# Kernel tuning notes

Measured on AMD Instinct MI355X. Metric: run time of the kernel, lower is better.

Reference implementation:

```python
import jax, jax.numpy as jnp
import numpy as np
import math

HEADS = 8
GROUPS = 4
PW = 2  # pooling_window
EPS = 1e-5


def group_norm(x, w, b, groups=GROUPS):
    # x: (B, C, *spatial); normalize over (C//groups, *spatial) per group
    B, C = x.shape[0], x.shape[1]
    xs = x.reshape(B, groups, -1)
    mu = xs.mean(-1, keepdims=True)
    var = xs.var(-1, keepdims=True)
    xs = (xs - mu) / jnp.sqrt(var + EPS)
    shape = (1, C) + (1,) * (x.ndim - 2)
    return xs.reshape(x.shape) * w.reshape(shape) + b.reshape(shape)


def cst_pool(x, pw=PW):
    # x: (B, C, Tq, Ts) with Ts = h*w + 1 (class token first); avg-pool spatial part
    cls_tok, sp = x[..., :1], x[..., 1:]
    B, C, Tq, S = sp.shape
    h = math.isqrt(S)
    sp = sp.reshape(B, C, Tq, h // pw, pw, h // pw, pw).mean(axis=(4, 6))
    return jnp.concatenate([cls_tok, sp.reshape(B, C, Tq, -1)], axis=-1)


def conv1x1(x, w):
    # w: (O, C); x: (B, C, Tq, Ts)
    return jnp.einsum('oc,bcqs->boqs', w, x)


def interp_bilinear_ac(m, n):
    # bilinear resize to (n, n), align_corners=True; m: (B, H, W) float
    def axis_interp(x, size, axis, L):
        c = jnp.linspace(0.0, L - 1.0, size)
        i0 = jnp.floor(c).astype(jnp.int32)
        i1 = jnp.minimum(i0 + 1, L - 1)
        f = (c - i0).astype(x.dtype)
        x0 = jnp.take(x, i0, axis=axis)
        x1 = jnp.take(x, i1, axis=axis)
        shape = [1] * x.ndim
        shape[axis] = size
        f = f.reshape(shape)
        return x0 * (1 - f) + x1 * f
    B, H, W = m.shape
    return axis_interp(axis_interp(m, n, 1, H), n, 2, W)


def setup_inputs() -> dict:
    key = jax.random.key(0)
    ks = jax.random.split(key, 8)
    B, Cin, Tq, Ts = 4, 128, 256, 257
    Cout = 512
    hidden = Cout // 2  # 256
    H = W = 256
    s = 0.05
    return {
        'corr_tokens': jax.random.normal(ks[0], (B, Cin, Tq, Ts), jnp.float32),
        's_masks': jax.random.randint(ks[1], (B, H, W), 0, 2, jnp.int32),
        'W_sc': jax.random.normal(ks[2], (Cout, Cin), jnp.float32) * s,
        'gn_sc_w': jnp.ones((Cout,), jnp.float32),
        'gn_sc_b': jnp.zeros((Cout,), jnp.float32),
        'W_qkv': jax.random.normal(ks[3], (3 * hidden, Cin), jnp.float32) * s,
        'b_qkv': jax.random.normal(ks[4], (3 * hidden,), jnp.float32) * s,
        'gn1_w': jnp.ones((hidden,), jnp.float32),
        'gn1_b': jnp.zeros((hidden,), jnp.float32),
        'W_agg': jax.random.normal(ks[5], (Cout, hidden), jnp.float32) * s,
        'gn2_w': jnp.ones((Cout,), jnp.float32),
        'gn2_b': jnp.zeros((Cout,), jnp.float32),
        'gn_out_w': jnp.ones((Cout,), jnp.float32),
        'gn_out_b': jnp.zeros((Cout,), jnp.float32),
    }


def reference(corr_tokens, s_masks, W_sc, gn_sc_w, gn_sc_b, W_qkv, b_qkv,
              gn1_w, gn1_b, W_agg, gn2_w, gn2_b, gn_out_w, gn_out_b):
    B, _, Tq, Ts = corr_tokens.shape
    hidden = W_qkv.shape[0] // 3
    E = hidden // HEADS

    # short_cut branch: conv1x1 -> CSTPooling -> GroupNorm -> ReLU
    residual = jax.nn.relu(group_norm(cst_pool(conv1x1(corr_tokens, W_sc)), gn_sc_w, gn_sc_b))

    # qkv projection
    qkv = conv1x1(corr_tokens, W_qkv) + b_qkv[None, :, None, None]
    qkv = qkv.reshape(B, 3, HEADS, E, Tq, Ts)  # channel order (x, g, e)
    q, k, v = qkv[:, 0], qkv[:, 1], qkv[:, 2]

    # pool queries over support-spatial dim: (B,G,E,Tq,Ts) -> (B,G,E,Tq,Td)
    q = cst_pool(q.reshape(B, hidden, Tq, Ts))
    Td = q.shape[-1]
    q = q.reshape(B, HEADS, E, Tq, Td)

    # per-query masked attention
    attn = jnp.einsum('bgeqd,bgeqs->bgqds', q, k)  # (B,G,Tq,Td,Ts)
    sdim = math.isqrt(Ts - 1)
    m = interp_bilinear_ac(jnp.minimum(s_masks, 1).astype(jnp.float32), sdim)
    m = m.reshape(B, 1, 1, 1, sdim * sdim)
    attn_seg = jnp.where(m == 0, jnp.float32(-1e9), attn[..., 1:])
    attn = jnp.concatenate([attn[..., :1], attn_seg], axis=-1)
    attn = jax.nn.softmax(attn, axis=-1)
    out = jnp.einsum('bgqds,bgeqs->bgeqd', attn, v).reshape(B, hidden, Tq, Td)

    # agg: GN -> ReLU -> conv1x1 -> GN -> ReLU
    out = jax.nn.relu(group_norm(out, gn1_w, gn1_b))
    out = conv1x1(out, W_agg)
    out = jax.nn.relu(group_norm(out, gn2_w, gn2_b))

    return group_norm(out + residual, gn_out_w, gn_out_b)
```

## Files before the change

### kernel.cpp

```cpp
#include <hip/hip_runtime.h>
#include <stdint.h>

#define NB    4
#define TQ    256
#define TS    257
#define TD    65
#define NPIX  16640
#define NPADQ 264
#define NPAD  67584
#define COUT  512
#define HID   256

typedef __attribute__((ext_vector_type(8))) short bf16x8;
typedef __attribute__((ext_vector_type(4))) float f32x4;

__device__ __forceinline__ float bf2f(unsigned short u) {
    union { unsigned int i; float f; } v; v.i = ((unsigned int)u) << 16; return v.f;
}
__device__ __forceinline__ unsigned short f2bf(float x) {
    union { float f; unsigned int i; } v; v.f = x;
    unsigned int r = v.i + 0x7fffu + ((v.i >> 16) & 1u);
    return (unsigned short)(r >> 16);
}

__device__ __forceinline__ float2 gn_params(const float* st, int bg, float invcnt) {
    float mu  = st[bg * 2] * invcnt;
    float var = st[bg * 2 + 1] * invcnt - mu * mu;
    float2 r; r.x = mu; r.y = rsqrtf(var + 1e-5f); return r;
}

__global__ void wprep_kernel(const float* __restrict__ wq, const float* __restrict__ wsc,
                             const float* __restrict__ wagg, unsigned short* __restrict__ wb) {
    int i = blockIdx.x * 256 + threadIdx.x;
    float v;
    if (i < 98304) v = wq[i];
    else if (i < 163840) v = wsc[i - 98304];
    else v = wagg[i - 163840];
    wb[i] = f2bf(v);
}

__global__ void mask_kernel(const int* __restrict__ sm, float* __restrict__ bias) {
    int b = blockIdx.x; int t = threadIdx.x;
    if (t >= 272) return;
    float v;
    if (t == 0) v = 0.0f;
    else if (t <= 256) {
        int s = t - 1; int i = s >> 4, j = s & 15;
        v = (sm[(size_t)b * 65536 + i * 17 * 256 + j * 17] != 0) ? 0.0f : -1e9f;
    } else v = -1e9f;
    bias[b * 272 + t] = v;
}

__global__ __launch_bounds__(256) void tpool_kernel(
    const float* __restrict__ corr,
    unsigned short* __restrict__ corrT,
    unsigned short* __restrict__ corrpT)
{
    int q = blockIdx.x, ch = blockIdx.y, b = blockIdx.z;
    int t = threadIdx.x;
    __shared__ unsigned short sT[264 * 66];

    {
        int laneT = t & 63; int crow = t >> 6;
        for (int c = crow; c < 64; c += 4) {
            const float* src = corr + (((size_t)b * 128 + ch * 64 + c) * 256 + q) * 257;
            for (int s = laneT; s < 257; s += 64) sT[s * 66 + c] = f2bf(src[s]);
        }
    }
    for (int idx = t; idx < 7 * 66; idx += 256) {
        int s = 257 + idx / 66, c = idx % 66;
        sT[s * 66 + c] = 0;
    }
    __syncthreads();

    {
        unsigned int* dst = (unsigned int*)corrT;
        size_t base = (size_t)b * (NPAD * 64) + (size_t)q * (264 * 64) + ch * 32;
        for (int idx = t; idx < 264 * 32; idx += 256) {
            int s = idx >> 5, cu = idx & 31;
            unsigned int v = (unsigned int)sT[s * 66 + 2 * cu] |
                             ((unsigned int)sT[s * 66 + 2 * cu + 1] << 16);
            dst[base + (size_t)s * 64 + cu] = v;
        }
    }
    {
        unsigned int* dst = (unsigned int*)corrpT;
        size_t base = (size_t)b * (NPIX * 64) + (size_t)q * (65 * 64) + ch * 32;
        for (int idx = t; idx < 65 * 32; idx += 256) {
            int d = idx >> 5, cu = idx & 31;
            float x0, x1;
            if (d == 0) {
                x0 = bf2f(sT[0 * 66 + 2 * cu]); x1 = bf2f(sT[0 * 66 + 2 * cu + 1]);
            } else {
                int dd = d - 1; int i = dd >> 3, j = dd & 7;
                int s = 1 + i * 32 + j * 2;
                int c0 = 2 * cu, c1 = 2 * cu + 1;
                x0 = 0.25f * (bf2f(sT[s*66+c0]) + bf2f(sT[(s+1)*66+c0]) +
                              bf2f(sT[(s+16)*66+c0]) + bf2f(sT[(s+17)*66+c0]));
                x1 = 0.25f * (bf2f(sT[s*66+c1]) + bf2f(sT[(s+1)*66+c1]) +
                              bf2f(sT[(s+16)*66+c1]) + bf2f(sT[(s+17)*66+c1]));
            }
            unsigned int v = (unsigned int)f2bf(x0) | ((unsigned int)f2bf(x1) << 16);
            dst[base + (size_t)d * 64 + cu] = v;
        }
    }
}

template<int MODE, int KT>
__global__ __launch_bounds__(256) void mgemm_kernel(
    const unsigned short* __restrict__ X,
    const unsigned short* __restrict__ Wb,
    int Nn,
    float* __restrict__ Yf,
    unsigned short* __restrict__ Y16,
    unsigned short* __restrict__ kb,
    unsigned short* __restrict__ vb,
    const float* __restrict__ bias,
    const float* __restrict__ st, const float* __restrict__ gw, const float* __restrict__ gb,
    float invcnt)
{
    int b  = blockIdx.z;
    int n0 = blockIdx.x * 128;
    int m0 = blockIdx.y * 128;
    int t = threadIdx.x;
    int w = t >> 6, lane = t & 63;
    int lm = lane & 15, lg = lane >> 4;
    int wn = (w & 1) * 64, wm = (w >> 1) * 64;

    __shared__ __align__(16) unsigned short sX[16384];
    __shared__ __align__(16) unsigned short sW[16384];

    f32x4 acc[4][4];
    #pragma unroll
    for (int i = 0; i < 4; i++)
        #pragma unroll
        for (int j = 0; j < 4; j++) { acc[i][j][0]=0.f; acc[i][j][1]=0.f; acc[i][j][2]=0.f; acc[i][j][3]=0.f; }

    for (int kc = 0; kc < KT / 128; kc++) {
        for (int i = t; i < 2048; i += 256) {
            int r_ = i >> 4, kq = i & 15;
            uint4 xv = *(const uint4*)&X[((size_t)b * Nn + n0 + r_) * KT + kc * 128 + (kq << 3)];
            if (MODE == 3) {
                union { uint4 v; unsigned short us[8]; } u; u.v = xv;
                int c0 = kc * 128 + (kq << 3);
                float2 p = gn_params(st, b * 4 + (c0 >> 6), invcnt);
                #pragma unroll
                for (int jj = 0; jj < 8; jj++) {
                    int cc = c0 + jj;
                    float v = bf2f(u.us[jj]);
                    v = fmaxf((v - p.x) * p.y * gw[cc] + gb[cc], 0.0f);
                    u.us[jj] = f2bf(v);
                }
                xv = u.v;
            }
            *(uint4*)&sX[r_ * 128 + ((kq ^ (r_ & 15)) << 3)] = xv;
            uint4 wv = *(const uint4*)&Wb[((size_t)(m0 + r_)) * KT + kc * 128 + (kq << 3)];
            *(uint4*)&sW[r_ * 128 + ((kq ^ (r_ & 15)) << 3)] = wv;
        }
        __syncthreads();
        #pragma unroll
        for (int kk = 0; kk < 4; kk++) {
            int kg = (kk << 2) | lg;
            bf16x8 af[4], bw[4];
            #pragma unroll
            for (int ii = 0; ii < 4; ii++)
                af[ii] = *(const bf16x8*)&sX[(wn + ii * 16 + lm) * 128 + ((kg ^ lm) << 3)];
            #pragma unroll
            for (int jj = 0; jj < 4; jj++)
                bw[jj] = *(const bf16x8*)&sW[(wm + jj * 16 + lm) * 128 + ((kg ^ lm) << 3)];
            #pragma unroll
            for (int ii = 0; ii < 4; ii++)
                #pragma unroll
                for (int jj = 0; jj < 4; jj++) {
                    if (MODE == 0)
                        acc[ii][jj] = __builtin_amdgcn_mfma_f32_16x16x32_bf16(bw[jj], af[ii], acc[ii][jj], 0,0,0);
                    else
                        acc[ii][jj] = __builtin_amdgcn_mfma_f32_16x16x32_bf16(af[ii], bw[jj], acc[ii][jj], 0,0,0);
                }
        }
        __syncthreads();
    }

    if (MODE == 0) {
        #pragma unroll
        for (int ii = 0; ii < 4; ii++) {
            int n = n0 + wn + ii * 16 + lm;
            #pragma unroll
            for (int jj = 0; jj < 4; jj++) {
                int mb = m0 + wm + jj * 16 + lg * 4;
                union { unsigned short us[4]; uint2 v; } pk;
                #pragma unroll
                for (int r = 0; r < 4; r++) pk.us[r] = f2bf(acc[ii][jj][r] + bias[mb + r]);
                *(uint2*)&Y16[((size_t)b * NPIX + n) * 256 + mb] = pk.v;
            }
        }
    } else if (MODE == 1) {
        if (m0 < 256) {
            #pragma unroll
            for (int ii = 0; ii < 4; ii++) {
                #pragma unroll
                for (int r = 0; r < 4; r++) {
                    unsigned int np = (unsigned int)(n0 + wn + ii * 16 + lg * 4 + r);
                    unsigned int qq = np / 264u;
                    unsigned int s  = np - qq * 264u;
                    #pragma unroll
                    for (int jj = 0; jj < 4; jj++) {
                        int m = m0 + wm + jj * 16 + lm;
                        int gch = m >> 5, e = m & 31;
                        kb[(((size_t)(b * 8 + gch) * 256 + qq) * 264 + s) * 32 + e] =
                            f2bf(acc[ii][jj][r] + bias[m]);
                    }
                }
            }
        } else {
            #pragma unroll
            for (int ii = 0; ii < 4; ii++) {
                int nb = n0 + wn + ii * 16 + lg * 4;
                #pragma unroll
                for (int jj = 0; jj < 4; jj++) {
                    int m = m0 + wm + jj * 16 + lm;
                    int mv = m - 256;
                    union { unsigned short us[4]; uint2 v; } pk;
                    #pragma unroll
                    for (int r = 0; r < 4; r++) pk.us[r] = f2bf(acc[ii][jj][r] + bias[m]);
                    *(uint2*)&vb[((size_t)b * 256 + mv) * NPAD + nb] = pk.v;
                }
            }
        }
    } else {
        #pragma unroll
        for (int ii = 0; ii < 4; ii++) {
            int nb = n0 + wn + ii * 16 + lg * 4;
            #pragma unroll
            for (int jj = 0; jj < 4; jj++) {
                int m = m0 + wm + jj * 16 + lm;
                *(f32x4*)&Yf[((size_t)b * COUT + m) * NPIX + nb] = acc[ii][jj];
            }
        }
    }
}

__global__ __launch_bounds__(320, 3) void attn_kernel(
    const unsigned short* __restrict__ kb,
    const unsigned short* __restrict__ vb,
    const unsigned short* __restrict__ qpT,
    const float* __restrict__ bias272,
    unsigned short* __restrict__ attT)
{
    int g = blockIdx.x, q = blockIdx.y, b = blockIdx.z;
    int t = threadIdx.x;
    int w = t >> 6, lane = t & 63;
    int lm = lane & 15, lg = lane >> 4;

    __shared__ __align__(16) unsigned short sP[23040];
    unsigned short* sPw = sP + w * 4608;

    int d = w * 16 + lm;
    int dc = d < 64 ? d : 64;
    bf16x8 qa = *(const bf16x8*)&qpT[((size_t)b * NPIX + q * 65 + dc) * 256 + g * 32 + lg * 8];
    if (d >= TD) { bf16x8 z = {}; qa = z; }

    size_t kb0 = ((size_t)(b * 8 + g) * 256 + q) * (264 * 32);
    const unsigned short* kp = kb + kb0 + (size_t)lm * 32 + lg * 8;
    bf16x8 kf[17];
    #pragma unroll
    for (int tt = 0; tt < 17; tt++)
        kf[tt] = *(const bf16x8*)&kp[tt * 512];

    f32x4 zero4 = {0.f, 0.f, 0.f, 0.f};
    f32x4 c[17];
    #pragma unroll
    for (int tt = 0; tt < 17; tt++)
        c[tt] = __builtin_amdgcn_mfma_f32_16x16x32_bf16(kf[tt], qa, zero4, 0, 0, 0);

    size_t vb0 = ((size_t)b * 256 + g * 32) * NPAD + (size_t)q * 264;
    const unsigned short* vp = vb + vb0 + (size_t)lm * NPAD + lg * 8;
    bf16x8 vf0[9], vf1[9];
    #pragma unroll
    for (int kk = 0; kk < 9; kk++) {
        vf0[kk] = *(const bf16x8*)&vp[kk * 32];
        vf1[kk] = *(const bf16x8*)&vp[16 * NPAD + kk * 32];
    }

    const float* bp = bias272 + b * 272 + lg * 4;
    #pragma unroll
    for (int tt = 0; tt < 17; tt++) {
        f32x4 bf = *(const f32x4*)&bp[tt * 16];
        c[tt][0] += bf[0]; c[tt][1] += bf[1]; c[tt][2] += bf[2]; c[tt][3] += bf[3];
    }

    f32x4 mv = c[0];
    #pragma unroll
    for (int tt = 1; tt < 17; tt++) {
        mv[0] = fmaxf(mv[0], c[tt][0]); mv[1] = fmaxf(mv[1], c[tt][1]);
        mv[2] = fmaxf(mv[2], c[tt][2]); mv[3] = fmaxf(mv[3], c[tt][3]);
    }
    float mx = fmaxf(fmaxf(mv[0], mv[1]), fmaxf(mv[2], mv[3]));
    mx = fmaxf(mx, __shfl_xor(mx, 16));
    mx = fmaxf(mx, __shfl_xor(mx, 32));
    float sm = 0.f;
    #pragma unroll
    for (int tt = 0; tt < 17; tt++) {
        #pragma unroll
        for (int r = 0; r < 4; r++) { float e_ = __expf(c[tt][r] - mx); c[tt][r] = e_; sm += e_; }
    }
    sm += __shfl_xor(sm, 16);
    sm += __shfl_xor(sm, 32);
    float inv = 1.0f / sm;

    #pragma unroll
    for (int tt = 0; tt < 17; tt++) {
        union { unsigned short us[4]; uint2 v; } pk;
        #pragma unroll
        for (int r = 0; r < 4; r++) pk.us[r] = f2bf(c[tt][r] * inv);
        int sg = tt * 2 + (lg >> 1);
        int off = lm * 288 + ((sg ^ (lm & 3)) << 3) + (lg & 1) * 4;
        *(uint2*)&sPw[off] = pk.v;
    }
    if (lg < 2) {
        int sg = 34 + lg;
        uint4 z4 = {0u, 0u, 0u, 0u};
        *(uint4*)&sPw[lm * 288 + ((sg ^ (lm & 3)) << 3)] = z4;
    }

    f32x4 o0 = zero4, o1 = zero4;
    #pragma unroll
    for (int kk = 0; kk < 9; kk++) {
        int kg = kk * 4 + lg;
        bf16x8 pa = *(const bf16x8*)&sPw[lm * 288 + ((kg ^ (lm & 3)) << 3)];
        o0 = __builtin_amdgcn_mfma_f32_16x16x32_bf16(pa, vf0[kk], o0, 0, 0, 0);
        o1 = __builtin_amdgcn_mfma_f32_16x16x32_bf16(pa, vf1[kk], o1, 0, 0, 0);
    }
    #pragma unroll
    for (int r = 0; r < 4; r++) {
        int dd = w * 16 + lg * 4 + r;
        if (dd < TD) {
            size_t nn = (size_t)b * NPIX + q * 65 + dd;
            attT[nn * 256 + g * 32 + lm]      = f2bf(o0[r]);
            attT[nn * 256 + g * 32 + 16 + lm] = f2bf(o1[r]);
        }
    }
}

__global__ void stats1_kernel(const unsigned short* __restrict__ attT, float* __restrict__ st) {
    int b = blockIdx.y;
    int t = threadIdx.x;
    int e8 = t & 31, g = e8 >> 3;
    int lane = t & 63;
    float s = 0.f, ss = 0.f;
    for (int r = blockIdx.x * 8 + (t >> 5); r < NPIX; r += gridDim.x * 8) {
        union { uint4 v; unsigned short us[8]; } u;
        u.v = *(const uint4*)&attT[((size_t)b * NPIX + r) * 256 + e8 * 8];
        #pragma unroll
        for (int j = 0; j < 8; j++) { float x = bf2f(u.us[j]); s += x; ss += x * x; }
    }
    s += __shfl_down(s, 32); ss += __shfl_down(ss, 32);
    s += __shfl_down(s, 4);  ss += __shfl_down(ss, 4);
    s += __shfl_down(s, 2);  ss += __shfl_down(ss, 2);
    s += __shfl_down(s, 1);  ss += __shfl_down(ss, 1);
    if (lane < 32 && (lane & 7) == 0) {
        atomicAdd(&st[(b * 4 + g) * 2],     s);
        atomicAdd(&st[(b * 4 + g) * 2 + 1], ss);
    }
}

__global__ void stats_kernel(const float* __restrict__ x, float* __restrict__ st, int Cg) {
    size_t len = (size_t)Cg * NPIX;
    size_t base = (size_t)blockIdx.y * len;
    const float4* x4 = reinterpret_cast<const float4*>(x + base);
    size_t len4 = len >> 2;
    float s = 0.f, ss = 0.f;
    for (size_t i = (size_t)blockIdx.x * blockDim.x + threadIdx.x; i < len4;
         i += (size_t)gridDim.x * blockDim.x) {
        float4 v = x4[i];
        s  += v.x + v.y + v.z + v.w;
        ss += v.x * v.x + v.y * v.y + v.z * v.z + v.w * v.w;
    }
    #pragma unroll
    for (int o = 32; o > 0; o >>= 1) { s += __shfl_down(s, o, 64); ss += __shfl_down(ss, o, 64); }
    __shared__ float red[4][2];
    int wid = threadIdx.x >> 6, lane = threadIdx.x & 63;
    if (lane == 0) { red[wid][0] = s; red[wid][1] = ss; }
    __syncthreads();
    if (threadIdx.x == 0) {
        float S  = red[0][0] + red[1][0] + red[2][0] + red[3][0];
        float SS = red[0][1] + red[1][1] + red[2][1] + red[3][1];
        atomicAdd(&st[blockIdx.y * 2],     S);
        atomicAdd(&st[blockIdx.y * 2 + 1], SS);
    }
}

__global__ void z_kernel(float* __restrict__ out, const float* __restrict__ scr,
                         const float* __restrict__ st2, const float* __restrict__ stsc,
                         const float* __restrict__ g2w, const float* __restrict__ g2b,
                         const float* __restrict__ gsw, const float* __restrict__ gsb)
{
    const float invcnt = 1.0f / (128.0f * NPIX);
    size_t total4 = (size_t)NB * COUT * (NPIX / 4);
    float4* o4 = reinterpret_cast<float4*>(out);
    const float4* s4 = reinterpret_cast<const float4*>(scr);
    for (size_t i = (size_t)blockIdx.x * blockDim.x + threadIdx.x; i < total4;
         i += (size_t)gridDim.x * blockDim.x) {
        size_t flat = i * 4;
        int c = (int)((flat / NPIX) % COUT);
        int b = (int)(flat / ((size_t)COUT * NPIX));
        int bg = b * 4 + (c >> 7);
        float2 p2 = gn_params(st2,  bg, invcnt);
        float2 ps = gn_params(stsc, bg, invcnt);
        float w2 = g2w[c] * p2.y, b2 = g2b[c] - p2.x * p2.y * g2w[c];
        float wsc = gsw[c] * ps.y, bsc = gsb[c] - ps.x * ps.y * gsw[c];
        float4 a = o4[i], r = s4[i], z;
        z.x = fmaxf(a.x * w2 + b2, 0.f) + fmaxf(r.x * wsc + bsc, 0.f);
        z.y = fmaxf(a.y * w2 + b2, 0.f) + fmaxf(r.y * wsc + bsc, 0.f);
        z.z = fmaxf(a.z * w2 + b2, 0.f) + fmaxf(r.z * wsc + bsc, 0.f);
        z.w = fmaxf(a.w * w2 + b2, 0.f) + fmaxf(r.w * wsc + bsc, 0.f);
        o4[i] = z;
    }
}

__global__ void norm_kernel(float* __restrict__ out, const float* __restrict__ st3,
                            const float* __restrict__ gw, const float* __restrict__ gb)
{
    const float invcnt = 1.0f / (128.0f * NPIX);
    size_t total4 = (size_t)NB * COUT * (NPIX / 4);
    float4* o4 = reinterpret_cast<float4*>(out);
    for (size_t i = (size_t)blockIdx.x * blockDim.x + threadIdx.x; i < total4;
         i += (size_t)gridDim.x * blockDim.x) {
        size_t flat = i * 4;
        int c = (int)((flat / NPIX) % COUT);
        int b = (int)(flat / ((size_t)COUT * NPIX));
        int bg = b * 4 + (c >> 7);
        float2 p = gn_params(st3, bg, invcnt);
        float w_ = gw[c] * p.y, b_ = gb[c] - p.x * p.y * gw[c];
        float4 a = o4[i], z;
        z.x = a.x * w_ + b_; z.y = a.y * w_ + b_; z.z = a.z * w_ + b_; z.w = a.w * w_ + b_;
        o4[i] = z;
    }
}

extern "C" void kernel_launch(void* const* d_in, const int* in_sizes, int n_in,
                              void* d_out, int out_size, void* d_ws, size_t ws_size,
                              hipStream_t stream) {
    (void)in_sizes; (void)n_in; (void)out_size; (void)ws_size;
    const float* corr     = (const float*)d_in[0];
    const int*   smask    = (const int*)  d_in[1];
    const float* W_sc     = (const float*)d_in[2];
    const float* gn_sc_w  = (const float*)d_in[3];
    const float* gn_sc_b  = (const float*)d_in[4];
    const float* W_qkv    = (const float*)d_in[5];
    const float* b_qkv    = (const float*)d_in[6];
    const float* gn1_w    = (const float*)d_in[7];
    const float* gn1_b    = (const float*)d_in[8];
    const float* W_agg    = (const float*)d_in[9];
    const float* gn2_w    = (const float*)d_in[10];
    const float* gn2_b    = (const float*)d_in[11];
    const float* gn_out_w = (const float*)d_in[12];
    const float* gn_out_b = (const float*)d_in[13];
    float* out = (float*)d_out;

    unsigned short* ws = (unsigned short*)d_ws;
    unsigned short* corrT  = ws;
    unsigned short* kbuf   = corrT  + (size_t)34603008;
    unsigned short* vbuf   = kbuf   + (size_t)69206016;
    unsigned short* corrpT = vbuf   + (size_t)69206016;
    unsigned short* qpT    = corrpT + (size_t)8519680;
    unsigned short* attT   = qpT    + (size_t)17039360;
    unsigned short* wbuf   = attT   + (size_t)17039360;
    float* bias  = (float*)(wbuf + (size_t)294912);
    float* stats = bias + 1088;
    float* scr   = (float*)d_ws;
    float* st_sc = stats, *st1 = stats + 32, *st2 = stats + 64, *st3 = stats + 96;

    const float inv1 = 1.0f / (64.0f * (float)NPIX);

    hipMemsetAsync(stats, 0, 128 * sizeof(float), stream);
    wprep_kernel<<<dim3(1152), dim3(256), 0, stream>>>(W_qkv, W_sc, W_agg, wbuf);
    mask_kernel<<<dim3(NB), dim3(320), 0, stream>>>(smask, bias);
    tpool_kernel<<<dim3(TQ, 2, NB), dim3(256), 0, stream>>>(corr, corrT, corrpT);
    mgemm_kernel<0,128><<<dim3(130, 2, NB), dim3(256), 0, stream>>>(
        corrpT, wbuf, NPIX, nullptr, qpT, nullptr, nullptr, b_qkv,
        nullptr, nullptr, nullptr, 0.f);
    mgemm_kernel<1,128><<<dim3(528, 4, NB), dim3(256), 0, stream>>>(
        corrT, wbuf + 32768, NPAD, nullptr, nullptr, kbuf, vbuf, b_qkv + 256,
        nullptr, nullptr, nullptr, 0.f);
    attn_kernel<<<dim3(8, TQ, NB), dim3(320), 0, stream>>>(kbuf, vbuf, qpT, bias, attT);
    stats1_kernel<<<dim3(208, NB), dim3(256), 0, stream>>>(attT, st1);
    mgemm_kernel<3,256><<<dim3(130, 4, NB), dim3(256), 0, stream>>>(
        attT, wbuf + 163840, NPIX, out, nullptr, nullptr, nullptr, nullptr,
        st1, gn1_w, gn1_b, inv1);
    stats_kernel<<<dim3(64, 16), dim3(256), 0, stream>>>(out, st2, 128);
    mgemm_kernel<2,128><<<dim3(130, 4, NB), dim3(256), 0, stream>>>(
        corrpT, wbuf + 98304, NPIX, scr, nullptr, nullptr, nullptr, nullptr,
        nullptr, nullptr, nullptr, 0.f);
    stats_kernel<<<dim3(64, 16), dim3(256), 0, stream>>>(scr, st_sc, 128);
    z_kernel<<<dim3(4096), dim3(256), 0, stream>>>(out, scr, st2, st_sc, gn2_w, gn2_b, gn_sc_w, gn_sc_b);
    stats_kernel<<<dim3(64, 16), dim3(256), 0, stream>>>(out, st3, 128);
    norm_kernel<<<dim3(4096), dim3(256), 0, stream>>>(out, st3, gn_out_w, gn_out_b);
}
```

Before: 1.059 ms.

## Stage K/V tiles through LDS via direct global-to-LDS loads, keep P in registers

The attention kernel used to have every wave load its own K and V fragments straight from global memory into registers. It now loads the shared K/V tile once per block into swizzled LDS using global_load_lds, with out-of-range rows read from a zero pad buffer. The softmax probabilities are no longer staged in LDS: they are packed with v_cvt_pk_bf16_f32 and rearranged across lanes with permlane32_swap and shuffles. Normalisation is deferred until after the PV product. This cuts redundant global loads across the five waves and the LDS round-trip for P, at the cost of a block-wide barrier and a dependence on a zero region inside corrT.

After: 982.4 us. 1.08x faster.

```diff
diff --git a/kernel.cpp b/kernel.cpp
--- a/kernel.cpp
+++ b/kernel.cpp
@@ -27,6 +27,13 @@
     float mu  = st[bg * 2] * invcnt;
     float var = st[bg * 2 + 1] * invcnt - mu * mu;
     float2 r; r.x = mu; r.y = rsqrtf(var + 1e-5f); return r;
+}
+
+__device__ __forceinline__ void gld_lds16(const void* g, void* l) {
+    __builtin_amdgcn_global_load_lds(
+        (const __attribute__((address_space(1))) unsigned int*)(size_t)g,
+        (__attribute__((address_space(3))) unsigned int*)(unsigned int)(size_t)l,
+        16, 0, 0);
 }
 
 __global__ void wprep_kernel(const float* __restrict__ wq, const float* __restrict__ wsc,
@@ -244,6 +251,7 @@
     const unsigned short* __restrict__ kb,
     const unsigned short* __restrict__ vb,
     const unsigned short* __restrict__ qpT,
+    const unsigned short* __restrict__ zpad,
     const float* __restrict__ bias272,
     unsigned short* __restrict__ attT)
 {
@@ -252,8 +260,8 @@
     int w = t >> 6, lane = t & 63;
     int lm = lane & 15, lg = lane >> 4;
 
-    __shared__ __align__(16) unsigned short sP[23040];
-    unsigned short* sPw = sP + w * 4608;
+    __shared__ __align__(16) unsigned short sbuf[17920];
+    const int VB = 8704;
 
     int d = w * 16 + lm;
     int dc = d < 64 ? d : 64;
@@ -261,25 +269,35 @@
     if (d >= TD) { bf16x8 z = {}; qa = z; }
 
     size_t kb0 = ((size_t)(b * 8 + g) * 256 + q) * (264 * 32);
-    const unsigned short* kp = kb + kb0 + (size_t)lm * 32 + lg * 8;
-    bf16x8 kf[17];
-    #pragma unroll
-    for (int tt = 0; tt < 17; tt++)
-        kf[tt] = *(const bf16x8*)&kp[tt * 512];
+    size_t vrow0 = (size_t)b * 256 + g * 32;
+    for (int cc = w; cc < 35; cc += 5) {
+        unsigned o = cc * 1024 + lane * 16;
+        const unsigned short* src;
+        if (cc < 17) {
+            unsigned mr = o >> 8, sl = (o >> 4) & 15;
+            unsigned lam = (o & ~0xF0u) | ((sl ^ (mr & 15)) << 4);
+            src = (lam < 16896u) ? (kb + kb0 + (lam >> 1)) : zpad;
+        } else {
+            unsigned ov = o - 17408u;
+            unsigned mr = ov >> 8, sl = (ov >> 4) & 15;
+            unsigned lam = (ov & ~0xF0u) | ((sl ^ (mr & 15)) << 4);
+            unsigned kk = lam >> 11, ch = (lam >> 6) & 31;
+            unsigned s = kk * 32 + ((lam >> 4) & 3) * 8;
+            src = (s < 264u) ? (vb + ((vrow0 + ch) * NPAD + (size_t)q * 264 + s)) : zpad;
+        }
+        gld_lds16(src, &sbuf[cc * 512]);
+    }
+    asm volatile("s_waitcnt vmcnt(0)" ::: "memory");
+    __syncthreads();
 
     f32x4 zero4 = {0.f, 0.f, 0.f, 0.f};
     f32x4 c[17];
-    #pragma unroll
-    for (int tt = 0; tt < 17; tt++)
-        c[tt] = __builtin_amdgcn_mfma_f32_16x16x32_bf16(kf[tt], qa, zero4, 0, 0, 0);
-
-    size_t vb0 = ((size_t)b * 256 + g * 32) * NPAD + (size_t)q * 264;
-    const unsigned short* vp = vb + vb0 + (size_t)lm * NPAD + lg * 8;
-    bf16x8 vf0[9], vf1[9];
-    #pragma unroll
-    for (int kk = 0; kk < 9; kk++) {
-        vf0[kk] = *(const bf16x8*)&vp[kk * 32];
-        vf1[kk] = *(const bf16x8*)&vp[16 * NPAD + kk * 32];
+    int sl0 = ((lm & 3) << 2) | lg;
+    #pragma unroll
+    for (int tt = 0; tt < 17; tt++) {
+        int mr = tt * 4 + (lm >> 2);
+        bf16x8 kf = *(const bf16x8*)&sbuf[mr * 128 + ((sl0 ^ (mr & 15)) << 3)];
+        c[tt] = __builtin_amdgcn_mfma_f32_16x16x32_bf16(kf, qa, zero4, 0, 0, 0);
     }
 
     const float* bp = bias272 + b * 272 + lg * 4;
@@ -308,36 +326,46 @@
     sm += __shfl_xor(sm, 32);
     float inv = 1.0f / sm;
 
+    unsigned plo[17], phi[17];
     #pragma unroll
     for (int tt = 0; tt < 17; tt++) {
-        union { unsigned short us[4]; uint2 v; } pk;
-        #pragma unroll
-        for (int r = 0; r < 4; r++) pk.us[r] = f2bf(c[tt][r] * inv);
-        int sg = tt * 2 + (lg >> 1);
-        int off = lm * 288 + ((sg ^ (lm & 3)) << 3) + (lg & 1) * 4;
-        *(uint2*)&sPw[off] = pk.v;
-    }
-    if (lg < 2) {
-        int sg = 34 + lg;
-        uint4 z4 = {0u, 0u, 0u, 0u};
-        *(uint4*)&sPw[lm * 288 + ((sg ^ (lm & 3)) << 3)] = z4;
-    }
-
+        asm("v_cvt_pk_bf16_f32 %0, %1, %2" : "=v"(plo[tt]) : "v"(c[tt][0]), "v"(c[tt][1]));
+        asm("v_cvt_pk_bf16_f32 %0, %1, %2" : "=v"(phi[tt]) : "v"(c[tt][2]), "v"(c[tt][3]));
+    }
+
+    bool lgEven = (lane & 16) == 0;
     f32x4 o0 = zero4, o1 = zero4;
     #pragma unroll
     for (int kk = 0; kk < 9; kk++) {
-        int kg = kk * 4 + lg;
-        bf16x8 pa = *(const bf16x8*)&sPw[lm * 288 + ((kg ^ (lm & 3)) << 3)];
-        o0 = __builtin_amdgcn_mfma_f32_16x16x32_bf16(pa, vf0[kk], o0, 0, 0, 0);
-        o1 = __builtin_amdgcn_mfma_f32_16x16x32_bf16(pa, vf1[kk], o1, 0, 0, 0);
-    }
+        unsigned A = plo[2 * kk];
+        unsigned C = phi[2 * kk];
+        unsigned B = (2 * kk + 1 < 17) ? plo[2 * kk + 1] : 0u;
+        unsigned D = (2 * kk + 1 < 17) ? phi[2 * kk + 1] : 0u;
+        asm("v_permlane32_swap_b32 %0, %1" : "+v"(A), "+v"(B));
+        asm("v_permlane32_swap_b32 %0, %1" : "+v"(C), "+v"(D));
+        unsigned Ax = __shfl_xor(A, 16), Bx = __shfl_xor(B, 16);
+        unsigned Cx = __shfl_xor(C, 16), Dx = __shfl_xor(D, 16);
+        union { unsigned u[4]; bf16x8 v; } pa;
+        pa.u[0] = lgEven ? A  : Bx;
+        pa.u[1] = lgEven ? C  : Dx;
+        pa.u[2] = lgEven ? Ax : B;
+        pa.u[3] = lgEven ? Cx : D;
+        int mr0 = kk * 8 + (lm >> 2), mr1 = mr0 + 4;
+        bf16x8 v0 = *(const bf16x8*)&sbuf[VB + mr0 * 128 + ((sl0 ^ (mr0 & 15)) << 3)];
+        bf16x8 v1 = *(const bf16x8*)&sbuf[VB + mr1 * 128 + ((sl0 ^ (mr1 & 15)) << 3)];
+        o0 = __builtin_amdgcn_mfma_f32_16x16x32_bf16(pa.v, v0, o0, 0, 0, 0);
+        o1 = __builtin_amdgcn_mfma_f32_16x16x32_bf16(pa.v, v1, o1, 0, 0, 0);
+    }
+    float invr[4];
+    #pragma unroll
+    for (int r = 0; r < 4; r++) invr[r] = __shfl(inv, lg * 4 + r);
     #pragma unroll
     for (int r = 0; r < 4; r++) {
         int dd = w * 16 + lg * 4 + r;
         if (dd < TD) {
             size_t nn = (size_t)b * NPIX + q * 65 + dd;
-            attT[nn * 256 + g * 32 + lm]      = f2bf(o0[r]);
-            attT[nn * 256 + g * 32 + 16 + lm] = f2bf(o1[r]);
+            attT[nn * 256 + g * 32 + lm]      = f2bf(o0[r] * invr[r]);
+            attT[nn * 256 + g * 32 + 16 + lm] = f2bf(o1[r] * invr[r]);
         }
     }
 }
@@ -483,7 +511,8 @@
     mgemm_kernel<1,128><<<dim3(528, 4, NB), dim3(256), 0, stream>>>(
         corrT, wbuf + 32768, NPAD, nullptr, nullptr, kbuf, vbuf, b_qkv + 256,
         nullptr, nullptr, nullptr, 0.f);
-    attn_kernel<<<dim3(8, TQ, NB), dim3(320), 0, stream>>>(kbuf, vbuf, qpT, bias, attT);
+    attn_kernel<<<dim3(8, TQ, NB), dim3(320), 0, stream>>>(
+        kbuf, vbuf, qpT, corrT + 32896, bias, attT);
     stats1_kernel<<<dim3(208, NB), dim3(256), 0, stream>>>(attT, st1);
     mgemm_kernel<3,256><<<dim3(130, 4, NB), dim3(256), 0, stream>>>(
         attT, wbuf + 163840, NPIX, out, nullptr, nullptr, nullptr, nullptr,
```
